# Performance work log

Measured on AMD Instinct MI355X. Metric: run time of the kernel, lower is better.

Reference implementation:

```python
import jax, jax.numpy as jnp
import numpy as np

N_LAYERS = 3
H = 128
N_NODES = 10000
N_EDGES = 160000
EPS = 1e-5

def silu(x):
    return x * jax.nn.sigmoid(x)

def batchnorm(x, gamma, beta):
    # BatchNorm1d, training-mode statistics (biased variance), over the node/edge dim
    mu = x.mean(axis=0)
    var = x.var(axis=0)
    return gamma * (x - mu) * jax.lax.rsqrt(var + EPS) + beta

def _forward(edge_index, emb_nodes, emb_edges, pre_Wn, pre_bn, pre_We, pre_be,
             We1, be1, We2, be2, Wx1, bx1, Wx2, bx2, Wh1, bh1, Wh2, bh2,
             gam_n, bet_n, gam_e, bet_e):
    src, dst = edge_index[0], edge_index[1]
    N = emb_nodes.shape[0]
    coords = emb_nodes                      # [N, 3] equivariant coordinates
    V = emb_nodes @ pre_Wn + pre_bn         # [N, H]
    E = emb_edges @ pre_We + pre_be         # [Ne, H] (overwritten by mij each layer)
    for l in range(N_LAYERS):
        diff = coords[dst] - coords[src]                          # [Ne, 3]
        dist = jnp.sqrt(jnp.sum(diff * diff, axis=-1, keepdims=True))  # [Ne, 1]
        h = jnp.concatenate([V[src], V[dst], dist, emb_edges], axis=-1)  # [Ne, 2H+3]
        mij = silu(silu(h @ We1[l] + be1[l]) @ We2[l] + be2[l])   # phi_e -> [Ne, H]
        px = silu(mij @ Wx1[l] + bx1[l]) @ Wx2[l] + bx2[l]        # phi_x -> [Ne, 3]
        # equivariant coordinate update; graph_node_index is None -> M = N
        coords = coords + jax.ops.segment_sum(diff * px, dst, num_segments=N) / (N - 1)
        mi = jax.ops.segment_sum(mij, dst, num_segments=N)        # [N, H]
        V = silu(jnp.concatenate([V, mi], axis=-1) @ Wh1[l] + bh1[l]) @ Wh2[l] + bh2[l]
        E = mij
        # encoder: act -> BatchNorm -> Dropout(eval = identity)
        V = batchnorm(jax.nn.elu(V), gam_n[l], bet_n[l])
        E = batchnorm(jax.nn.elu(E), gam_e[l], bet_e[l])
    return V, E

def setup_inputs() -> dict:
    key = jax.random.key(0)
    ks = iter(jax.random.split(key, 32))
    def rn(shape, scale=0.05):
        return jax.random.normal(next(ks), shape, dtype=jnp.float32) * scale
    src = jax.random.randint(next(ks), (N_EDGES,), 0, N_NODES)
    off = jax.random.randint(next(ks), (N_EDGES,), 1, N_NODES)
    dst = (src + off) % N_NODES  # no self-loops -> distance never exactly 0
    edge_index = jnp.stack([src, dst]).astype(jnp.int64) if jax.config.jax_enable_x64 else jnp.stack([src, dst])
    return dict(
        emb_nodes=jax.random.normal(next(ks), (N_NODES, 3), dtype=jnp.float32),
        emb_edges=jax.random.normal(next(ks), (N_EDGES, 2), dtype=jnp.float32),
        edge_index=edge_index,
        pre_Wn=rn((3, H)), pre_bn=jnp.zeros((H,), jnp.float32),
        pre_We=rn((2, H)), pre_be=jnp.zeros((H,), jnp.float32),
        We1=rn((N_LAYERS, 2 * H + 3, H)), be1=jnp.zeros((N_LAYERS, H), jnp.float32),
        We2=rn((N_LAYERS, H, H)), be2=jnp.zeros((N_LAYERS, H), jnp.float32),
        Wx1=rn((N_LAYERS, H, H)), bx1=jnp.zeros((N_LAYERS, H), jnp.float32),
        Wx2=rn((N_LAYERS, H, 3)), bx2=jnp.zeros((N_LAYERS, 3), jnp.float32),
        Wh1=rn((N_LAYERS, 2 * H, H)), bh1=jnp.zeros((N_LAYERS, H), jnp.float32),
        Wh2=rn((N_LAYERS, H, H)), bh2=jnp.zeros((N_LAYERS, H), jnp.float32),
        gam_n=jnp.ones((N_LAYERS, H), jnp.float32), bet_n=jnp.zeros((N_LAYERS, H), jnp.float32),
        gam_e=jnp.ones((N_LAYERS, H), jnp.float32), bet_e=jnp.zeros((N_LAYERS, H), jnp.float32),
    )

def reference(emb_nodes, emb_edges, edge_index, pre_Wn, pre_bn, pre_We, pre_be,
              We1, be1, We2, be2, Wx1, bx1, Wx2, bx2, Wh1, bh1, Wh2, bh2,
              gam_n, bet_n, gam_e, bet_e):
    return _forward(edge_index, emb_nodes, emb_edges, pre_Wn, pre_bn, pre_We, pre_be,
                    We1, be1, We2, be2, Wx1, bx1, Wx2, bx2, Wh1, bh1, Wh2, bh2,
                    gam_n, bet_n, gam_e, bet_e)
```

## Files before the change

kernel.cpp:

```cpp
#include <hip/hip_runtime.h>
#include <hip/hip_bf16.h>
#include <math.h>

#define NN 10000
#define NE 160000
#define HH 128
#define EPSBN 1e-5f

static constexpr int NT = 256;

typedef __attribute__((ext_vector_type(8))) short s8b;
typedef __attribute__((ext_vector_type(4))) float f32x4;

#define MFMA16 __builtin_amdgcn_mfma_f32_16x16x32_bf16

__device__ __forceinline__ float silu_f(float x) { return x / (1.f + __expf(-x)); }
__device__ __forceinline__ float elu_f(float x)  { return x > 0.f ? x : expm1f(x); }

__device__ __forceinline__ ushort rnb(float x) {
    unsigned u = __float_as_uint(x);
    unsigned r = (u + 0x7fffu + ((u >> 16) & 1u)) >> 16;
    return (ushort)r;
}
__device__ __forceinline__ float bf2f(ushort u) {
    return __uint_as_float(((unsigned)u) << 16);
}
__device__ __forceinline__ s8b ldg8(const ushort* p) { return *(const s8b*)p; }

__global__ void k_zero(float* __restrict__ p, int n) {
    int i = blockIdx.x * blockDim.x + threadIdx.x;
    if (i < n) p[i] = 0.f;
}
__global__ void k_zero_int(int* __restrict__ p, int n) {
    int i = blockIdx.x * blockDim.x + threadIdx.x;
    if (i < n) p[i] = 0;
}
__global__ void k_copy(const float* __restrict__ a, float* __restrict__ b, int n) {
    int i = blockIdx.x * blockDim.x + threadIdx.x;
    if (i < n) b[i] = a[i];
}

__global__ void k_vinit(const float* __restrict__ en, const float* __restrict__ Wn,
                        const float* __restrict__ bn, ushort* __restrict__ Vb) {
    int idx = blockIdx.x * blockDim.x + threadIdx.x;
    if (idx >= NN * HH) return;
    int i = idx >> 7, j = idx & 127;
    float v = fmaf(en[i * 3 + 0], Wn[j], bn[j]);
    v = fmaf(en[i * 3 + 1], Wn[HH + j], v);
    v = fmaf(en[i * 3 + 2], Wn[2 * HH + j], v);
    Vb[idx] = rnb(v);
}

__global__ void k_wprep(const float* __restrict__ We1, const float* __restrict__ We2,
                        const float* __restrict__ Wx1, const float* __restrict__ Wh1,
                        const float* __restrict__ Wh2, ushort* __restrict__ Wb) {
    int idx = blockIdx.x * 256 + threadIdx.x;
    if (idx >= 344064) return;
    int layer = idx / 114688;
    int r = idx - layer * 114688;
    const float* src; int K; int roff;
    if (r < 32768)      { src = We1 + (size_t)layer * 33152; K = 256; roff = r; }
    else if (r < 49152) { src = We2 + (size_t)layer * 16384; K = 128; roff = r - 32768; }
    else if (r < 65536) { src = Wx1 + (size_t)layer * 16384; K = 128; roff = r - 49152; }
    else if (r < 98304) { src = Wh1 + (size_t)layer * 32768; K = 256; roff = r - 65536; }
    else                { src = Wh2 + (size_t)layer * 16384; K = 128; roff = r - 98304; }
    int n = roff / K, k = roff - n * K;
    Wb[idx] = rnb(src[k * 128 + n]);
}

__global__ void k_hist(const int* __restrict__ dst, int* __restrict__ deg) {
    int e = blockIdx.x * blockDim.x + threadIdx.x;
    if (e < NE) atomicAdd(&deg[dst[e]], 1);
}
__global__ __launch_bounds__(256)
void k_scan(const int* __restrict__ deg, int* __restrict__ offs, int* __restrict__ cur) {
    __shared__ int part[256];
    const int t = threadIdx.x;
    const int s0 = t * 40, s1 = min(s0 + 40, NN);
    int s = 0;
    for (int i = s0; i < s1; ++i) s += deg[i];
    part[t] = s;
    __syncthreads();
    if (t == 0) {
        int r = 0;
        for (int i = 0; i < 256; ++i) { int v = part[i]; part[i] = r; r += v; }
    }
    __syncthreads();
    int r = part[t];
    for (int i = s0; i < s1; ++i) { offs[i] = r; cur[i] = r; r += deg[i]; }
    if (t == 255) offs[NN] = r;
}
__global__ void k_fill(const int* __restrict__ dst, int* __restrict__ cur, int* __restrict__ eid) {
    int e = blockIdx.x * blockDim.x + threadIdx.x;
    if (e < NE) {
        int p = atomicAdd(&cur[dst[e]], 1);
        eid[p] = e;
    }
}

__global__ void k_eprep(const float* __restrict__ coords, const int* __restrict__ src,
                        const int* __restrict__ dst, float4* __restrict__ diff4) {
    int e = blockIdx.x * blockDim.x + threadIdx.x;
    if (e >= NE) return;
    int s = src[e], d = dst[e];
    float dx = coords[d * 3 + 0] - coords[s * 3 + 0];
    float dy = coords[d * 3 + 1] - coords[s * 3 + 1];
    float dz = coords[d * 3 + 2] - coords[s * 3 + 2];
    float dist = sqrtf(dx * dx + dy * dy + dz * dz);
    diff4[e] = make_float4(dx, dy, dz, dist);
}

__global__ __launch_bounds__(256, 5)
void k_efused(const ushort* __restrict__ Vb,
              const int* __restrict__ src, const int* __restrict__ dst,
              const float4* __restrict__ diff4, const float* __restrict__ ee,
              const ushort* __restrict__ W1b,
              const float* __restrict__ We1f, const float* __restrict__ be1,
              const ushort* __restrict__ W2b,
              const float* __restrict__ be2, ushort* __restrict__ mijb) {
    __shared__ ushort t1b[4][64][40];
    __shared__ int sid[64], did[64];
    __shared__ float dd[64], eAa[64], eBb[64];
    const int t = threadIdx.x;
    const int lane = t & 63;
    const int w = t >> 6;
    const int wr = w >> 1, wc = w & 1;
    const int e0 = blockIdx.x * 64;
    if (t < 64) {
        int e = e0 + t;
        sid[t] = src[e]; did[t] = dst[e];
        float4 q = diff4[e];
        dd[t] = q.w; eAa[t] = ee[2 * e]; eBb[t] = ee[2 * e + 1];
    }
    __syncthreads();
    const int l15 = lane & 15, lq = lane >> 4;
    f32x4 acc[2][4];
#pragma unroll
    for (int i = 0; i < 2; ++i)
#pragma unroll
        for (int j = 0; j < 4; ++j) acc[i][j] = (f32x4){0.f, 0.f, 0.f, 0.f};

#pragma unroll
    for (int half = 0; half < 2; ++half) {
        const int* ids = half ? did : sid;
#pragma unroll
        for (int kt = 0; kt < 4; ++kt) {
            const int wk = half * 128 + kt * 32;
            s8b a[2], b[4];
#pragma unroll
            for (int mi = 0; mi < 2; ++mi) {
                int row = ids[wr * 32 + mi * 16 + l15];
                a[mi] = ldg8(Vb + (size_t)row * HH + kt * 32 + lq * 8);
            }
#pragma unroll
            for (int ni = 0; ni < 4; ++ni) {
                int col = wc * 64 + ni * 16 + l15;
                b[ni] = ldg8(W1b + (size_t)col * 256 + wk + lq * 8);
            }
#pragma unroll
            for (int mi = 0; mi < 2; ++mi)
#pragma unroll
                for (int ni = 0; ni < 4; ++ni)
                    acc[mi][ni] = MFMA16(a[mi], b[ni], acc[mi][ni], 0, 0, 0);
        }
    }
#pragma unroll
    for (int mi = 0; mi < 2; ++mi)
#pragma unroll
        for (int ni = 0; ni < 4; ++ni) {
            int col = wc * 64 + ni * 16 + l15;
            float w256 = We1f[256 * HH + col];
            float w257 = We1f[257 * HH + col];
            float w258 = We1f[258 * HH + col];
            float bi = be1[col];
            int kt = col >> 5, c = col & 31;
#pragma unroll
            for (int r = 0; r < 4; ++r) {
                int m = wr * 32 + mi * 16 + lq * 4 + r;
                float v = acc[mi][ni][r] + bi;
                v = fmaf(dd[m], w256, v);
                v = fmaf(eAa[m], w257, v);
                v = fmaf(eBb[m], w258, v);
                t1b[kt][m][c] = rnb(silu_f(v));
                acc[mi][ni][r] = 0.f;
            }
        }
    __syncthreads();
#pragma unroll
    for (int kt = 0; kt < 4; ++kt) {
        s8b a[2], b[4];
#pragma unroll
        for (int mi = 0; mi < 2; ++mi) {
            int row = wr * 32 + mi * 16 + l15;
            a[mi] = *(const s8b*)&t1b[kt][row][lq * 8];
        }
#pragma unroll
        for (int ni = 0; ni < 4; ++ni) {
            int col = wc * 64 + ni * 16 + l15;
            b[ni] = ldg8(W2b + (size_t)col * 128 + kt * 32 + lq * 8);
        }
#pragma unroll
        for (int mi = 0; mi < 2; ++mi)
#pragma unroll
            for (int ni = 0; ni < 4; ++ni)
                acc[mi][ni] = MFMA16(a[mi], b[ni], acc[mi][ni], 0, 0, 0);
    }
#pragma unroll
    for (int mi = 0; mi < 2; ++mi)
#pragma unroll
        for (int ni = 0; ni < 4; ++ni) {
            int col = wc * 64 + ni * 16 + l15;
            float bi = be2[col];
#pragma unroll
            for (int r = 0; r < 4; ++r) {
                int m = wr * 32 + mi * 16 + lq * 4 + r;
                mijb[(size_t)(e0 + m) * HH + col] = rnb(silu_f(acc[mi][ni][r] + bi));
            }
        }
}

__global__ __launch_bounds__(128)
void k_mi(const ushort* __restrict__ mijb, const int* __restrict__ offs,
          const int* __restrict__ eid, ushort* __restrict__ mib) {
    const int n = blockIdx.x;
    const int t = threadIdx.x;
    const int b = offs[n], e = offs[n + 1];
    float s = 0.f;
    for (int j = b; j < e; ++j)
        s += bf2f(mijb[(size_t)eid[j] * HH + t]);
    mib[(size_t)n * HH + t] = rnb(s);
}

__global__ __launch_bounds__(256, 4)
void k_egemm3(const ushort* __restrict__ mijb, const float4* __restrict__ diff4,
              const ushort* __restrict__ Bb,
              const float* __restrict__ bias, const float* __restrict__ W2,
              const float* __restrict__ b2, float4* __restrict__ cd4) {
    __shared__ float Ts[64][133];
    __shared__ float d3[3][64];
    __shared__ float Wxs[HH * 3];
    __shared__ float b2s[3];
    const int t = threadIdx.x;
    const int lane = t & 63;
    const int w = t >> 6;
    const int wr = w >> 1, wc = w & 1;
    const int e0 = blockIdx.x * 64;
    if (t < 64) {
        float4 q = diff4[e0 + t];
        d3[0][t] = q.x; d3[1][t] = q.y; d3[2][t] = q.z;
    }
    for (int i = t; i < HH * 3; i += NT) Wxs[i] = W2[i];
    if (t < 3) b2s[t] = b2[t];
    const int l15 = lane & 15, lq = lane >> 4;
    f32x4 acc[2][4];
#pragma unroll
    for (int i = 0; i < 2; ++i)
#pragma unroll
        for (int j = 0; j < 4; ++j) acc[i][j] = (f32x4){0.f, 0.f, 0.f, 0.f};

#pragma unroll
    for (int kt = 0; kt < 4; ++kt) {
        s8b a[2], b[4];
#pragma unroll
        for (int mi = 0; mi < 2; ++mi) {
            int row = e0 + wr * 32 + mi * 16 + l15;
            a[mi] = ldg8(mijb + (size_t)row * HH + kt * 32 + lq * 8);
        }
#pragma unroll
        for (int ni = 0; ni < 4; ++ni) {
            int col = wc * 64 + ni * 16 + l15;
            b[ni] = ldg8(Bb + (size_t)col * 128 + kt * 32 + lq * 8);
        }
#pragma unroll
        for (int mi = 0; mi < 2; ++mi)
#pragma unroll
            for (int ni = 0; ni < 4; ++ni)
                acc[mi][ni] = MFMA16(a[mi], b[ni], acc[mi][ni], 0, 0, 0);
    }
#pragma unroll
    for (int mi = 0; mi < 2; ++mi)
#pragma unroll
        for (int ni = 0; ni < 4; ++ni) {
            int col = wc * 64 + ni * 16 + l15;
            float bi = bias[col];
#pragma unroll
            for (int r = 0; r < 4; ++r) {
                int m = wr * 32 + mi * 16 + lq * 4 + r;
                Ts[m][col] = silu_f(acc[mi][ni][r] + bi);
            }
        }
    __syncthreads();
    if (t < 192) {
        int r = t / 3;
        int col = t - 3 * r;
        float s = b2s[col];
#pragma unroll 16
        for (int k = 0; k < HH; ++k)
            s = fmaf(Ts[r][k], Wxs[k * 3 + col], s);
        ((float*)&cd4[e0 + r])[col] = d3[col][r] * s;
    }
}

__global__ void k_coordupd(float* __restrict__ coords, const float4* __restrict__ cd4,
                           const int* __restrict__ offs, const int* __restrict__ eid) {
    int idx = blockIdx.x * blockDim.x + threadIdx.x;
    if (idx >= NN * 3) return;
    int n = idx / 3, c = idx - 3 * n;
    int b = offs[n], e = offs[n + 1];
    float s = 0.f;
    for (int j = b; j < e; ++j)
        s += ((const float*)&cd4[eid[j]])[c];
    coords[idx] += s * (1.f / (NN - 1));
}

__global__ __launch_bounds__(256, 4)
void k_ngemm1(const ushort* __restrict__ Vb, const ushort* __restrict__ mib,
              const ushort* __restrict__ Bb,
              const float* __restrict__ bias, ushort* __restrict__ ub) {
    const int t = threadIdx.x;
    const int lane = t & 63;
    const int w = t >> 6;
    const int wr = w >> 1, wc = w & 1;
    const int r0 = blockIdx.x * 64;
    const int l15 = lane & 15, lq = lane >> 4;
    f32x4 acc[2][4];
#pragma unroll
    for (int i = 0; i < 2; ++i)
#pragma unroll
        for (int j = 0; j < 4; ++j) acc[i][j] = (f32x4){0.f, 0.f, 0.f, 0.f};

#pragma unroll
    for (int kk = 0; kk < 8; ++kk) {
        const ushort* Ap = (kk < 4) ? Vb : mib;
        const int k0 = (kk & 3) * 32;
        s8b a[2], b[4];
#pragma unroll
        for (int mi_ = 0; mi_ < 2; ++mi_) {
            int row = r0 + wr * 32 + mi_ * 16 + l15;
            if (row >= NN) row = NN - 1;
            a[mi_] = ldg8(Ap + (size_t)row * HH + k0 + lq * 8);
        }
#pragma unroll
        for (int ni = 0; ni < 4; ++ni) {
            int col = wc * 64 + ni * 16 + l15;
            b[ni] = ldg8(Bb + (size_t)col * 256 + kk * 32 + lq * 8);
        }
#pragma unroll
        for (int mi_ = 0; mi_ < 2; ++mi_)
#pragma unroll
            for (int ni = 0; ni < 4; ++ni)
                acc[mi_][ni] = MFMA16(a[mi_], b[ni], acc[mi_][ni], 0, 0, 0);
    }
#pragma unroll
    for (int mi_ = 0; mi_ < 2; ++mi_)
#pragma unroll
        for (int ni = 0; ni < 4; ++ni) {
            int col = wc * 64 + ni * 16 + l15;
            float bi = bias[col];
#pragma unroll
            for (int r = 0; r < 4; ++r) {
                int m = r0 + wr * 32 + mi_ * 16 + lq * 4 + r;
                if (m < NN) ub[(size_t)m * HH + col] = rnb(silu_f(acc[mi_][ni][r] + bi));
            }
        }
}

__global__ __launch_bounds__(256, 4)
void k_ngemm2(const ushort* __restrict__ ub,
              const ushort* __restrict__ Bb,
              const float* __restrict__ bias, float* __restrict__ X,
              float* __restrict__ ssum, float* __restrict__ ssq) {
    const int t = threadIdx.x;
    const int lane = t & 63;
    const int w = t >> 6;
    const int wr = w >> 1, wc = w & 1;
    const int r0 = blockIdx.x * 64;
    const int l15 = lane & 15, lq = lane >> 4;
    f32x4 acc[2][4];
#pragma unroll
    for (int i = 0; i < 2; ++i)
#pragma unroll
        for (int j = 0; j < 4; ++j) acc[i][j] = (f32x4){0.f, 0.f, 0.f, 0.f};

#pragma unroll
    for (int kt = 0; kt < 4; ++kt) {
        s8b a[2], b[4];
#pragma unroll
        for (int mi_ = 0; mi_ < 2; ++mi_) {
            int row = r0 + wr * 32 + mi_ * 16 + l15;
            if (row >= NN) row = NN - 1;
            a[mi_] = ldg8(ub + (size_t)row * HH + kt * 32 + lq * 8);
        }
#pragma unroll
        for (int ni = 0; ni < 4; ++ni) {
            int col = wc * 64 + ni * 16 + l15;
            b[ni] = ldg8(Bb + (size_t)col * 128 + kt * 32 + lq * 8);
        }
#pragma unroll
        for (int mi_ = 0; mi_ < 2; ++mi_)
#pragma unroll
            for (int ni = 0; ni < 4; ++ni)
                acc[mi_][ni] = MFMA16(a[mi_], b[ni], acc[mi_][ni], 0, 0, 0);
    }
    float s[4] = {0.f, 0.f, 0.f, 0.f}, q[4] = {0.f, 0.f, 0.f, 0.f};
#pragma unroll
    for (int mi_ = 0; mi_ < 2; ++mi_)
#pragma unroll
        for (int ni = 0; ni < 4; ++ni) {
            int col = wc * 64 + ni * 16 + l15;
            float bi = bias[col];
#pragma unroll
            for (int r = 0; r < 4; ++r) {
                int m = r0 + wr * 32 + mi_ * 16 + lq * 4 + r;
                float v = elu_f(acc[mi_][ni][r] + bi);
                if (m < NN) {
                    X[(size_t)m * HH + col] = v;
                    s[ni] += v; q[ni] += v * v;
                }
            }
        }
#pragma unroll
    for (int j = 0; j < 4; ++j) {
        s[j] += __shfl_xor(s[j], 16);
        s[j] += __shfl_xor(s[j], 32);
        q[j] += __shfl_xor(q[j], 16);
        q[j] += __shfl_xor(q[j], 32);
    }
    if (lane < 16) {
#pragma unroll
        for (int j = 0; j < 4; ++j) {
            int col = wc * 64 + j * 16 + l15;
            atomicAdd(&ssum[col], s[j]);
            atomicAdd(&ssq[col], q[j]);
        }
    }
}

__global__ void k_bnorm_nodes(const float* __restrict__ X, const float* __restrict__ ssum,
                              const float* __restrict__ ssq, const float* __restrict__ gam,
                              const float* __restrict__ bet, float* __restrict__ outf,
                              ushort* __restrict__ outb, int writeb) {
    int idx = blockIdx.x * blockDim.x + threadIdx.x;
    if (idx >= NN * HH) return;
    int c = idx & 127;
    float mu = ssum[c] * (1.f / NN);
    float var = ssq[c] * (1.f / NN) - mu * mu;
    float v = fmaf(gam[c] * (X[idx] - mu), rsqrtf(var + EPSBN), bet[c]);
    if (writeb) outb[idx] = rnb(v);
    else        outf[idx] = v;
}

__global__ __launch_bounds__(256)
void k_estats(const ushort* __restrict__ mijb, float* __restrict__ ssum, float* __restrict__ ssq) {
    const int t = threadIdx.x;
    const int col = t & 127;
    const int half = t >> 7;
    const int rbase = blockIdx.x * 250;
    float s = 0.f, q = 0.f;
    for (int r = rbase + half; r < rbase + 250; r += 2) {
        float x = elu_f(bf2f(mijb[(size_t)r * HH + col]));
        s += x; q += x * x;
    }
    atomicAdd(&ssum[col], s);
    atomicAdd(&ssq[col], q);
}

__global__ void k_bnorm_edges(const ushort* __restrict__ mijb, const float* __restrict__ ssum,
                              const float* __restrict__ ssq, const float* __restrict__ gam,
                              const float* __restrict__ bet, float* __restrict__ out) {
    size_t stride = (size_t)gridDim.x * blockDim.x;
    for (size_t idx = (size_t)blockIdx.x * blockDim.x + threadIdx.x; idx < (size_t)NE * HH; idx += stride) {
        int c = (int)(idx & 127);
        float x = elu_f(bf2f(mijb[idx]));
        float mu = ssum[c] * (1.f / NE);
        float var = ssq[c] * (1.f / NE) - mu * mu;
        out[idx] = fmaf(gam[c] * (x - mu), rsqrtf(var + EPSBN), bet[c]);
    }
}

extern "C" void kernel_launch(void* const* d_in, const int* in_sizes, int n_in,
                              void* d_out, int out_size, void* d_ws, size_t ws_size,
                              hipStream_t stream) {
    (void)in_sizes; (void)n_in; (void)out_size; (void)ws_size;
    const float* emb_nodes = (const float*)d_in[0];
    const float* emb_edges = (const float*)d_in[1];
    const int*   eidx      = (const int*)d_in[2];
    const float* pre_Wn = (const float*)d_in[3];
    const float* pre_bn = (const float*)d_in[4];
    const float* We1 = (const float*)d_in[7];
    const float* be1 = (const float*)d_in[8];
    const float* We2 = (const float*)d_in[9];
    const float* be2 = (const float*)d_in[10];
    const float* Wx1 = (const float*)d_in[11];
    const float* bx1 = (const float*)d_in[12];
    const float* Wx2 = (const float*)d_in[13];
    const float* bx2 = (const float*)d_in[14];
    const float* Wh1 = (const float*)d_in[15];
    const float* bh1 = (const float*)d_in[16];
    const float* Wh2 = (const float*)d_in[17];
    const float* bh2 = (const float*)d_in[18];
    const float* gam_n = (const float*)d_in[19];
    const float* bet_n = (const float*)d_in[20];
    const float* gam_e = (const float*)d_in[21];
    const float* bet_e = (const float*)d_in[22];

    const int* src = eidx;
    const int* dst = eidx + NE;

    float* ws = (float*)d_ws;
    float*   coords = ws;
    float4*  diff4  = (float4*)(ws + 30000);
    ushort*  Vb     = (ushort*)(ws + 670000);
    ushort*  mib    = (ushort*)(ws + 1310000);
    ushort*  ub     = (ushort*)(ws + 1950000);
    float*   X      = ws + 2590000;
    float4*  cd4    = (float4*)(ws + 3870000);
    ushort*  mijb   = (ushort*)(ws + 4510000);
    float*   snN    = ws + 14750000;
    float*   sqN    = ws + 14750128;
    float*   snE    = ws + 14750256;
    float*   sqE    = ws + 14750384;
    ushort*  Wb     = (ushort*)(ws + 14750512);
    int*     I0     = (int*)(ws + 14922544);
    int*     deg    = I0;
    int*     offs   = I0 + 10000;
    int*     cur    = I0 + 20001;
    int*     eid    = I0 + 30001;

    float* outV = (float*)d_out;
    float* outE = (float*)d_out + (size_t)NN * HH;

    k_copy<<<(30000 + 255) / 256, 256, 0, stream>>>(emb_nodes, coords, 30000);
    k_vinit<<<(NN * HH + 255) / 256, 256, 0, stream>>>(emb_nodes, pre_Wn, pre_bn, Vb);
    k_wprep<<<1344, 256, 0, stream>>>(We1, We2, Wx1, Wh1, Wh2, Wb);

    k_zero_int<<<(NN + 255) / 256, 256, 0, stream>>>(deg, NN);
    k_hist<<<(NE + 255) / 256, 256, 0, stream>>>(dst, deg);
    k_scan<<<1, 256, 0, stream>>>(deg, offs, cur);
    k_fill<<<(NE + 255) / 256, 256, 0, stream>>>(dst, cur, eid);

    for (int l = 0; l < 3; ++l) {
        const float* We1l = We1 + (size_t)l * 259 * 128;
        const float* be1l = be1 + l * 128;
        const float* be2l = be2 + l * 128;
        const float* bx1l = bx1 + l * 128;
        const float* Wx2l = Wx2 + (size_t)l * 128 * 3;
        const float* bx2l = bx2 + l * 3;
        const float* bh1l = bh1 + l * 128;
        const float* bh2l = bh2 + l * 128;
        const size_t L = (size_t)l * 114688;
        const ushort* W1b = Wb + L;
        const ushort* W2b = Wb + L + 32768;
        const ushort* Wxb = Wb + L + 49152;
        const ushort* Whb = Wb + L + 65536;
        const ushort* Wgb = Wb + L + 98304;

        k_zero<<<2, 256, 0, stream>>>(snN, 512);
        k_eprep<<<(NE + 255) / 256, 256, 0, stream>>>(coords, src, dst, diff4);
        k_efused<<<NE / 64, NT, 0, stream>>>(Vb, src, dst, diff4, emb_edges,
                                             W1b, We1l, be1l, W2b, be2l, mijb);
        k_egemm3<<<NE / 64, NT, 0, stream>>>(mijb, diff4, Wxb, bx1l, Wx2l, bx2l, cd4);
        k_mi<<<NN, 128, 0, stream>>>(mijb, offs, eid, mib);
        k_coordupd<<<(NN * 3 + 255) / 256, 256, 0, stream>>>(coords, cd4, offs, eid);
        k_ngemm1<<<(NN + 63) / 64, NT, 0, stream>>>(Vb, mib, Whb, bh1l, ub);
        k_ngemm2<<<(NN + 63) / 64, NT, 0, stream>>>(ub, Wgb, bh2l, X, snN, sqN);
        k_bnorm_nodes<<<(NN * HH + 255) / 256, 256, 0, stream>>>(X, snN, sqN, gam_n + l * 128,
                                                                 bet_n + l * 128,
                                                                 outV, Vb, (l < 2) ? 1 : 0);
        if (l == 2) {
            k_estats<<<640, 256, 0, stream>>>(mijb, snE, sqE);
            k_bnorm_edges<<<4096, 256, 0, stream>>>(mijb, snE, sqE, gam_e + l * 128, bet_e + l * 128, outE);
        }
    }
}
```

Measured before the change: 870.7 us.

## Fuse edge prep, phi_x MLP into edge kernel and fuse node GEMMs

The edge kernel now takes 128 edges per 512-thread block. It computes diff and dist inline from coords, which removes k_eprep and the diff4 buffer. It then runs the phi_x MLP in place: mij is staged in shared memory and fed to a second MFMA GEMM, and the 128→3 projection uses a zero-padded bf16 MFMA tile, which removes k_egemm3 and its reread of mij. The two node GEMMs are also merged into one kernel that keeps the hidden activation in LDS instead of writing and rereading a ub buffer. The larger block and extra phases add shared-memory use and register pressure, and the px projection now runs in bf16 rather than fp32.

```diff
diff --git a/kernel.cpp b/kernel.cpp
--- a/kernel.cpp
+++ b/kernel.cpp
@@ -6,8 +6,6 @@
 #define NE 160000
 #define HH 128
 #define EPSBN 1e-5f
-
-static constexpr int NT = 256;
 
 typedef __attribute__((ext_vector_type(8))) short s8b;
 typedef __attribute__((ext_vector_type(4))) float f32x4;
@@ -68,6 +66,15 @@
     Wb[idx] = rnb(src[k * 128 + n]);
 }
 
+__global__ void k_wx2prep(const float* __restrict__ Wx2, ushort* __restrict__ Wx2b) {
+    int idx = blockIdx.x * 256 + threadIdx.x;
+    if (idx >= 3 * 16 * 128) return;
+    int layer = idx / 2048;
+    int r = idx - layer * 2048;
+    int n = r >> 7, k = r & 127;
+    Wx2b[idx] = (n < 3) ? rnb(Wx2[layer * 384 + k * 3 + n]) : (ushort)0;
+}
+
 __global__ void k_hist(const int* __restrict__ dst, int* __restrict__ deg) {
     int e = blockIdx.x * blockDim.x + threadIdx.x;
     if (e < NE) atomicAdd(&deg[dst[e]], 1);
@@ -98,39 +105,38 @@
     }
 }
 
-__global__ void k_eprep(const float* __restrict__ coords, const int* __restrict__ src,
-                        const int* __restrict__ dst, float4* __restrict__ diff4) {
-    int e = blockIdx.x * blockDim.x + threadIdx.x;
-    if (e >= NE) return;
-    int s = src[e], d = dst[e];
-    float dx = coords[d * 3 + 0] - coords[s * 3 + 0];
-    float dy = coords[d * 3 + 1] - coords[s * 3 + 1];
-    float dz = coords[d * 3 + 2] - coords[s * 3 + 2];
-    float dist = sqrtf(dx * dx + dy * dy + dz * dz);
-    diff4[e] = make_float4(dx, dy, dz, dist);
-}
-
-__global__ __launch_bounds__(256, 5)
+__global__ __launch_bounds__(512, 4)
 void k_efused(const ushort* __restrict__ Vb,
               const int* __restrict__ src, const int* __restrict__ dst,
-              const float4* __restrict__ diff4, const float* __restrict__ ee,
+              const float* __restrict__ coords, const float* __restrict__ ee,
               const ushort* __restrict__ W1b,
               const float* __restrict__ We1f, const float* __restrict__ be1,
               const ushort* __restrict__ W2b,
-              const float* __restrict__ be2, ushort* __restrict__ mijb) {
-    __shared__ ushort t1b[4][64][40];
-    __shared__ int sid[64], did[64];
-    __shared__ float dd[64], eAa[64], eBb[64];
+              const float* __restrict__ be2,
+              const ushort* __restrict__ Wxb,
+              const float* __restrict__ bx1,
+              const ushort* __restrict__ Wx2b,
+              const float* __restrict__ bx2,
+              ushort* __restrict__ mijb, float4* __restrict__ cd4) {
+    __shared__ ushort t1b[4][128][40];
+    __shared__ int sid[128], did[128];
+    __shared__ float dd[128], eAa[128], eBb[128];
+    __shared__ float d3[3][128];
     const int t = threadIdx.x;
     const int lane = t & 63;
     const int w = t >> 6;
     const int wr = w >> 1, wc = w & 1;
-    const int e0 = blockIdx.x * 64;
-    if (t < 64) {
+    const int e0 = blockIdx.x * 128;
+    if (t < 128) {
         int e = e0 + t;
-        sid[t] = src[e]; did[t] = dst[e];
-        float4 q = diff4[e];
-        dd[t] = q.w; eAa[t] = ee[2 * e]; eBb[t] = ee[2 * e + 1];
+        int s = src[e], d = dst[e];
+        sid[t] = s; did[t] = d;
+        float dx = coords[d * 3 + 0] - coords[s * 3 + 0];
+        float dy = coords[d * 3 + 1] - coords[s * 3 + 1];
+        float dz = coords[d * 3 + 2] - coords[s * 3 + 2];
+        dd[t] = sqrtf(dx * dx + dy * dy + dz * dz);
+        d3[0][t] = dx; d3[1][t] = dy; d3[2][t] = dz;
+        eAa[t] = ee[2 * e]; eBb[t] = ee[2 * e + 1];
     }
     __syncthreads();
     const int l15 = lane & 15, lq = lane >> 4;
@@ -205,18 +211,74 @@
             for (int ni = 0; ni < 4; ++ni)
                 acc[mi][ni] = MFMA16(a[mi], b[ni], acc[mi][ni], 0, 0, 0);
     }
+    __syncthreads();
 #pragma unroll
     for (int mi = 0; mi < 2; ++mi)
 #pragma unroll
         for (int ni = 0; ni < 4; ++ni) {
             int col = wc * 64 + ni * 16 + l15;
             float bi = be2[col];
+            int kt = col >> 5, c = col & 31;
 #pragma unroll
             for (int r = 0; r < 4; ++r) {
                 int m = wr * 32 + mi * 16 + lq * 4 + r;
-                mijb[(size_t)(e0 + m) * HH + col] = rnb(silu_f(acc[mi][ni][r] + bi));
-            }
-        }
+                ushort mv = rnb(silu_f(acc[mi][ni][r] + bi));
+                mijb[(size_t)(e0 + m) * HH + col] = mv;
+                t1b[kt][m][c] = mv;
+                acc[mi][ni][r] = 0.f;
+            }
+        }
+    __syncthreads();
+#pragma unroll
+    for (int kt = 0; kt < 4; ++kt) {
+        s8b a[2], b[4];
+#pragma unroll
+        for (int mi = 0; mi < 2; ++mi) {
+            int row = wr * 32 + mi * 16 + l15;
+            a[mi] = *(const s8b*)&t1b[kt][row][lq * 8];
+        }
+#pragma unroll
+        for (int ni = 0; ni < 4; ++ni) {
+            int col = wc * 64 + ni * 16 + l15;
+            b[ni] = ldg8(Wxb + (size_t)col * 128 + kt * 32 + lq * 8);
+        }
+#pragma unroll
+        for (int mi = 0; mi < 2; ++mi)
+#pragma unroll
+            for (int ni = 0; ni < 4; ++ni)
+                acc[mi][ni] = MFMA16(a[mi], b[ni], acc[mi][ni], 0, 0, 0);
+    }
+    __syncthreads();
+#pragma unroll
+    for (int mi = 0; mi < 2; ++mi)
+#pragma unroll
+        for (int ni = 0; ni < 4; ++ni) {
+            int col = wc * 64 + ni * 16 + l15;
+            float bi = bx1[col];
+            int kt = col >> 5, c = col & 31;
+#pragma unroll
+            for (int r = 0; r < 4; ++r) {
+                int m = wr * 32 + mi * 16 + lq * 4 + r;
+                t1b[kt][m][c] = rnb(silu_f(acc[mi][ni][r] + bi));
+            }
+        }
+    __syncthreads();
+    f32x4 accd = (f32x4){0.f, 0.f, 0.f, 0.f};
+#pragma unroll
+    for (int kt = 0; kt < 4; ++kt) {
+        s8b a = *(const s8b*)&t1b[kt][w * 16 + l15][lq * 8];
+        s8b b = ldg8(Wx2b + (size_t)l15 * 128 + kt * 32 + lq * 8);
+        accd = MFMA16(a, b, accd, 0, 0, 0);
+    }
+    if (l15 < 3) {
+        float bi = bx2[l15];
+#pragma unroll
+        for (int r = 0; r < 4; ++r) {
+            int row = w * 16 + lq * 4 + r;
+            float px = accd[r] + bi;
+            ((float*)&cd4[e0 + row])[l15] = d3[l15][row] * px;
+        }
+    }
 }
 
 __global__ __launch_bounds__(128)
@@ -231,76 +293,6 @@
     mib[(size_t)n * HH + t] = rnb(s);
 }
 
-__global__ __launch_bounds__(256, 4)
-void k_egemm3(const ushort* __restrict__ mijb, const float4* __restrict__ diff4,
-              const ushort* __restrict__ Bb,
-              const float* __restrict__ bias, const float* __restrict__ W2,
-              const float* __restrict__ b2, float4* __restrict__ cd4) {
-    __shared__ float Ts[64][133];
-    __shared__ float d3[3][64];
-    __shared__ float Wxs[HH * 3];
-    __shared__ float b2s[3];
-    const int t = threadIdx.x;
-    const int lane = t & 63;
-    const int w = t >> 6;
-    const int wr = w >> 1, wc = w & 1;
-    const int e0 = blockIdx.x * 64;
-    if (t < 64) {
-        float4 q = diff4[e0 + t];
-        d3[0][t] = q.x; d3[1][t] = q.y; d3[2][t] = q.z;
-    }
-    for (int i = t; i < HH * 3; i += NT) Wxs[i] = W2[i];
-    if (t < 3) b2s[t] = b2[t];
-    const int l15 = lane & 15, lq = lane >> 4;
-    f32x4 acc[2][4];
-#pragma unroll
-    for (int i = 0; i < 2; ++i)
-#pragma unroll
-        for (int j = 0; j < 4; ++j) acc[i][j] = (f32x4){0.f, 0.f, 0.f, 0.f};
-
-#pragma unroll
-    for (int kt = 0; kt < 4; ++kt) {
-        s8b a[2], b[4];
-#pragma unroll
-        for (int mi = 0; mi < 2; ++mi) {
-            int row = e0 + wr * 32 + mi * 16 + l15;
-            a[mi] = ldg8(mijb + (size_t)row * HH + kt * 32 + lq * 8);
-        }
-#pragma unroll
-        for (int ni = 0; ni < 4; ++ni) {
-            int col = wc * 64 + ni * 16 + l15;
-            b[ni] = ldg8(Bb + (size_t)col * 128 + kt * 32 + lq * 8);
-        }
-#pragma unroll
-        for (int mi = 0; mi < 2; ++mi)
-#pragma unroll
-            for (int ni = 0; ni < 4; ++ni)
-                acc[mi][ni] = MFMA16(a[mi], b[ni], acc[mi][ni], 0, 0, 0);
-    }
-#pragma unroll
-    for (int mi = 0; mi < 2; ++mi)
-#pragma unroll
-        for (int ni = 0; ni < 4; ++ni) {
-            int col = wc * 64 + ni * 16 + l15;
-            float bi = bias[col];
-#pragma unroll
-            for (int r = 0; r < 4; ++r) {
-                int m = wr * 32 + mi * 16 + lq * 4 + r;
-                Ts[m][col] = silu_f(acc[mi][ni][r] + bi);
-            }
-        }
-    __syncthreads();
-    if (t < 192) {
-        int r = t / 3;
-        int col = t - 3 * r;
-        float s = b2s[col];
-#pragma unroll 16
-        for (int k = 0; k < HH; ++k)
-            s = fmaf(Ts[r][k], Wxs[k * 3 + col], s);
-        ((float*)&cd4[e0 + r])[col] = d3[col][r] * s;
-    }
-}
-
 __global__ void k_coordupd(float* __restrict__ coords, const float4* __restrict__ cd4,
                            const int* __restrict__ offs, const int* __restrict__ eid) {
     int idx = blockIdx.x * blockDim.x + threadIdx.x;
@@ -313,10 +305,15 @@
     coords[idx] += s * (1.f / (NN - 1));
 }
 
-__global__ __launch_bounds__(256, 4)
-void k_ngemm1(const ushort* __restrict__ Vb, const ushort* __restrict__ mib,
-              const ushort* __restrict__ Bb,
-              const float* __restrict__ bias, ushort* __restrict__ ub) {
+__global__ __launch_bounds__(256, 5)
+void k_nfused(const ushort* __restrict__ Vb, const ushort* __restrict__ mib,
+              const ushort* __restrict__ Whb,
+              const float* __restrict__ bh1,
+              const ushort* __restrict__ Wgb,
+              const float* __restrict__ bh2,
+              float* __restrict__ X,
+              float* __restrict__ ssum, float* __restrict__ ssq) {
+    __shared__ ushort tb[4][64][40];
     const int t = threadIdx.x;
     const int lane = t & 63;
     const int w = t >> 6;
@@ -343,7 +340,7 @@
 #pragma unroll
         for (int ni = 0; ni < 4; ++ni) {
             int col = wc * 64 + ni * 16 + l15;
-            b[ni] = ldg8(Bb + (size_t)col * 256 + kk * 32 + lq * 8);
+            b[ni] = ldg8(Whb + (size_t)col * 256 + kk * 32 + lq * 8);
         }
 #pragma unroll
         for (int mi_ = 0; mi_ < 2; ++mi_)
@@ -356,45 +353,28 @@
 #pragma unroll
         for (int ni = 0; ni < 4; ++ni) {
             int col = wc * 64 + ni * 16 + l15;
-            float bi = bias[col];
+            float bi = bh1[col];
+            int kt = col >> 5, c = col & 31;
 #pragma unroll
             for (int r = 0; r < 4; ++r) {
-                int m = r0 + wr * 32 + mi_ * 16 + lq * 4 + r;
-                if (m < NN) ub[(size_t)m * HH + col] = rnb(silu_f(acc[mi_][ni][r] + bi));
-            }
-        }
-}
-
-__global__ __launch_bounds__(256, 4)
-void k_ngemm2(const ushort* __restrict__ ub,
-              const ushort* __restrict__ Bb,
-              const float* __restrict__ bias, float* __restrict__ X,
-              float* __restrict__ ssum, float* __restrict__ ssq) {
-    const int t = threadIdx.x;
-    const int lane = t & 63;
-    const int w = t >> 6;
-    const int wr = w >> 1, wc = w & 1;
-    const int r0 = blockIdx.x * 64;
-    const int l15 = lane & 15, lq = lane >> 4;
-    f32x4 acc[2][4];
-#pragma unroll
-    for (int i = 0; i < 2; ++i)
-#pragma unroll
-        for (int j = 0; j < 4; ++j) acc[i][j] = (f32x4){0.f, 0.f, 0.f, 0.f};
-
+                int m = wr * 32 + mi_ * 16 + lq * 4 + r;
+                tb[kt][m][c] = rnb(silu_f(acc[mi_][ni][r] + bi));
+                acc[mi_][ni][r] = 0.f;
+            }
+        }
+    __syncthreads();
 #pragma unroll
     for (int kt = 0; kt < 4; ++kt) {
         s8b a[2], b[4];
 #pragma unroll
         for (int mi_ = 0; mi_ < 2; ++mi_) {
-            int row = r0 + wr * 32 + mi_ * 16 + l15;
-            if (row >= NN) row = NN - 1;
-            a[mi_] = ldg8(ub + (size_t)row * HH + kt * 32 + lq * 8);
-        }
-#pragma unroll
-        for (int ni = 0; ni < 4; ++ni) {
-            int col = wc * 64 + ni * 16 + l15;
-            b[ni] = ldg8(Bb + (size_t)col * 128 + kt * 32 + lq * 8);
+            int row = wr * 32 + mi_ * 16 + l15;
+            a[mi_] = *(const s8b*)&tb[kt][row][lq * 8];
+        }
+#pragma unroll
+        for (int ni = 0; ni < 4; ++ni) {
+            int col = wc * 64 + ni * 16 + l15;
+            b[ni] = ldg8(Wgb + (size_t)col * 128 + kt * 32 + lq * 8);
         }
 #pragma unroll
         for (int mi_ = 0; mi_ < 2; ++mi_)
@@ -408,7 +388,7 @@
 #pragma unroll
         for (int ni = 0; ni < 4; ++ni) {
             int col = wc * 64 + ni * 16 + l15;
-            float bi = bias[col];
+            float bi = bh2[col];
 #pragma unroll
             for (int r = 0; r < 4; ++r) {
                 int m = r0 + wr * 32 + mi_ * 16 + lq * 4 + r;
@@ -509,19 +489,18 @@
 
     float* ws = (float*)d_ws;
     float*   coords = ws;
-    float4*  diff4  = (float4*)(ws + 30000);
-    ushort*  Vb     = (ushort*)(ws + 670000);
-    ushort*  mib    = (ushort*)(ws + 1310000);
-    ushort*  ub     = (ushort*)(ws + 1950000);
-    float*   X      = ws + 2590000;
-    float4*  cd4    = (float4*)(ws + 3870000);
-    ushort*  mijb   = (ushort*)(ws + 4510000);
-    float*   snN    = ws + 14750000;
-    float*   sqN    = ws + 14750128;
-    float*   snE    = ws + 14750256;
-    float*   sqE    = ws + 14750384;
-    ushort*  Wb     = (ushort*)(ws + 14750512);
-    int*     I0     = (int*)(ws + 14922544);
+    ushort*  Vb     = (ushort*)(ws + 30000);
+    ushort*  mib    = (ushort*)(ws + 670000);
+    float*   X      = ws + 1310000;
+    float4*  cd4    = (float4*)(ws + 2590000);
+    ushort*  mijb   = (ushort*)(ws + 3230000);
+    float*   snN    = ws + 13470000;
+    float*   sqN    = ws + 13470128;
+    float*   snE    = ws + 13470256;
+    float*   sqE    = ws + 13470384;
+    ushort*  Wb     = (ushort*)(ws + 13470512);
+    ushort*  Wx2b   = (ushort*)(ws + 13642544);
+    int*     I0     = (int*)(ws + 13645616);
     int*     deg    = I0;
     int*     offs   = I0 + 10000;
     int*     cur    = I0 + 20001;
@@ -533,6 +512,7 @@
     k_copy<<<(30000 + 255) / 256, 256, 0, stream>>>(emb_nodes, coords, 30000);
     k_vinit<<<(NN * HH + 255) / 256, 256, 0, stream>>>(emb_nodes, pre_Wn, pre_bn, Vb);
     k_wprep<<<1344, 256, 0, stream>>>(We1, We2, Wx1, Wh1, Wh2, Wb);
+    k_wx2prep<<<24, 256, 0, stream>>>(Wx2, Wx2b);
 
     k_zero_int<<<(NN + 255) / 256, 256, 0, stream>>>(deg, NN);
     k_hist<<<(NE + 255) / 256, 256, 0, stream>>>(dst, deg);
@@ -544,7 +524,6 @@
         const float* be1l = be1 + l * 128;
         const float* be2l = be2 + l * 128;
         const float* bx1l = bx1 + l * 128;
-        const float* Wx2l = Wx2 + (size_t)l * 128 * 3;
         const float* bx2l = bx2 + l * 3;
         const float* bh1l = bh1 + l * 128;
         const float* bh2l = bh2 + l * 128;
@@ -554,16 +533,15 @@
         const ushort* Wxb = Wb + L + 49152;
         const ushort* Whb = Wb + L + 65536;
         const ushort* Wgb = Wb + L + 98304;
+        const ushort* Wx2bl = Wx2b + (size_t)l * 2048;
 
         k_zero<<<2, 256, 0, stream>>>(snN, 512);
-        k_eprep<<<(NE + 255) / 256, 256, 0, stream>>>(coords, src, dst, diff4);
-        k_efused<<<NE / 64, NT, 0, stream>>>(Vb, src, dst, diff4, emb_edges,
-                                             W1b, We1l, be1l, W2b, be2l, mijb);
-        k_egemm3<<<NE / 64, NT, 0, stream>>>(mijb, diff4, Wxb, bx1l, Wx2l, bx2l, cd4);
+        k_efused<<<NE / 128, 512, 0, stream>>>(Vb, src, dst, coords, emb_edges,
+                                               W1b, We1l, be1l, W2b, be2l,
+                                               Wxb, bx1l, Wx2bl, bx2l, mijb, cd4);
         k_mi<<<NN, 128, 0, stream>>>(mijb, offs, eid, mib);
         k_coordupd<<<(NN * 3 + 255) / 256, 256, 0, stream>>>(coords, cd4, offs, eid);
-        k_ngemm1<<<(NN + 63) / 64, NT, 0, stream>>>(Vb, mib, Whb, bh1l, ub);
-        k_ngemm2<<<(NN + 63) / 64, NT, 0, stream>>>(ub, Wgb, bh2l, X, snN, sqN);
+        k_nfused<<<(NN + 63) / 64, 256, 0, stream>>>(Vb, mib, Whb, bh1l, Wgb, bh2l, X, snN, sqN);
         k_bnorm_nodes<<<(NN * HH + 255) / 256, 256, 0, stream>>>(X, snN, sqN, gam_n + l * 128,
                                                                  bet_n + l * 128,
                                                                  outV, Vb, (l < 2) ? 1 : 0);
```

New measurement: 852.2 us. 2.1% less time.
